# Kernel optimization log

Hardware: AMD Instinct MI355X
Metric: run time of the kernel (lower is better)

The kernel has to match this reference:

```python
import jax, jax.numpy as jnp
import numpy as np

N_NODES = 50000
N_EDGES = 600000
DIM = 128
N_LAYERS = 3
N_GRAPHS = 512
BN_EPS = 1e-5


def setup_inputs() -> dict:
    key = jax.random.key(0)
    ks = jax.random.split(key, 8)
    x = jax.random.normal(ks[0], (N_NODES, DIM), dtype=jnp.float32)
    edge_index = jax.random.randint(ks[1], (2, N_EDGES), 0, N_NODES, dtype=jnp.int32)
    batch = jnp.sort(jax.random.randint(ks[2], (N_NODES,), 0, N_GRAPHS, dtype=jnp.int32))
    W1s = jax.random.normal(ks[3], (N_LAYERS, DIM, DIM), dtype=jnp.float32) * (1.0 / np.sqrt(DIM))
    b1s = jnp.zeros((N_LAYERS, DIM), dtype=jnp.float32)
    W2s = jax.random.normal(ks[4], (N_LAYERS, DIM, DIM), dtype=jnp.float32) * (1.0 / np.sqrt(DIM))
    b2s = jnp.zeros((N_LAYERS, DIM), dtype=jnp.float32)
    gammas = jnp.ones((N_LAYERS, DIM), dtype=jnp.float32)
    betas = jnp.zeros((N_LAYERS, DIM), dtype=jnp.float32)
    return {"x": x, "edge_index": edge_index, "batch": batch,
            "W1s": W1s, "b1s": b1s, "W2s": W2s, "b2s": b2s,
            "gammas": gammas, "betas": betas}


def reference(x, edge_index, batch, W1s, b1s, W2s, b2s, gammas, betas):
    # EncoderGIN.forward: stack of GINConv (eps=0) -> ReLU -> BatchNorm1d (train mode),
    # then global_add_pool per layer and concat along feature dim.
    n_nodes = x.shape[0]
    src, dst = edge_index[0], edge_index[1]
    h = x
    pools = []
    for i in range(N_LAYERS):
        # GINConv: aggregate sum of neighbor feats at dst, add (1+0)*self
        agg = jax.ops.segment_sum(h[src], dst, num_segments=n_nodes) + h
        # MLP: Linear -> ReLU -> Linear
        h1 = jax.nn.relu(agg @ W1s[i] + b1s[i])
        h2 = h1 @ W2s[i] + b2s[i]
        # outer ReLU
        h2 = jax.nn.relu(h2)
        # BatchNorm1d, training mode (biased variance over the node dim)
        mean = jnp.mean(h2, axis=0)
        var = jnp.var(h2, axis=0)
        h = (h2 - mean) * jax.lax.rsqrt(var + BN_EPS) * gammas[i] + betas[i]
        pools.append(jax.ops.segment_sum(h, batch, num_segments=N_GRAPHS))
    return jnp.concatenate(pools, axis=1)  # [N_GRAPHS, N_LAYERS*DIM]
```

## Files before the change

kernel.cpp:

```cpp
#include <hip/hip_runtime.h>

#define N_NODES 50000
#define N_EDGES 600000
#define DIM 128
#define N_GRAPHS 512
#define N_LAYERS 3
#define OUT_STRIDE (N_LAYERS * DIM)
#define BN_EPS 1e-5f
#define N_REP 16
#define CAP 64

#define NPB 128
#define NBIN 391
#define BCAP_BIN 3072
#define PADC 16
#define EPB 4096
#define NB3 147

typedef __attribute__((ext_vector_type(8))) short short8;
typedef __attribute__((ext_vector_type(4))) float floatx4;

__device__ inline short f2bf(float f) {
    union { float f; unsigned u; } x{f};
    unsigned r = x.u + 0x7fffu + ((x.u >> 16) & 1u);
    return (short)(r >> 16);
}
__device__ inline float bf2f(short h) {
    union { unsigned u; float f; } x;
    x.u = ((unsigned)(unsigned short)h) << 16;
    return x.f;
}
__device__ inline void split_trunc(float f, short& hi, short& lo) {
    union { float f; unsigned u; } x{f};
    hi = (short)(x.u >> 16);
    union { unsigned u; float f; } hf;
    hf.u = x.u & 0xffff0000u;
    union { float f; unsigned u; } y{f - hf.f};
    lo = (short)(y.u >> 16);
}
__device__ inline floatx4 bf4_to_f4(uint2 w) {
    union { unsigned u; float f; } a, b, c, d;
    a.u = w.x << 16;
    b.u = w.x & 0xffff0000u;
    c.u = w.y << 16;
    d.u = w.y & 0xffff0000u;
    return floatx4{a.f, b.f, c.f, d.f};
}

__global__ __launch_bounds__(256) void prep_scatter_kernel(const int* __restrict__ src,
                                                           const int* __restrict__ dst,
                                                           int* __restrict__ binCur,
                                                           int2* __restrict__ binned,
                                                           const float* __restrict__ W1s,
                                                           const float* __restrict__ W2s,
                                                           short* __restrict__ Whi,
                                                           short* __restrict__ Wlo,
                                                           const float* __restrict__ x,
                                                           short* __restrict__ xb) {
    if (blockIdx.x < NB3) {
        __shared__ int hist[NBIN];
        __shared__ int basev[NBIN];
        const int t = threadIdx.x;
        for (int b = t; b < NBIN; b += 256) hist[b] = 0;
        __syncthreads();
        const int e0 = blockIdx.x * EPB;
        int sreg[16], dreg[16], rreg[16];
#pragma unroll
        for (int k = 0; k < 16; ++k) {
            int e = e0 + k * 256 + t;
            if (e < N_EDGES) {
                sreg[k] = src[e];
                dreg[k] = dst[e];
            } else {
                dreg[k] = -1;
            }
        }
#pragma unroll
        for (int k = 0; k < 16; ++k)
            if (dreg[k] >= 0) rreg[k] = atomicAdd(&hist[dreg[k] >> 7], 1);
        __syncthreads();
        for (int b = t; b < NBIN; b += 256) {
            int c = hist[b];
            basev[b] = (c > 0) ? atomicAdd(&binCur[b * PADC], c) : 0;
        }
        __syncthreads();
#pragma unroll
        for (int k = 0; k < 16; ++k)
            if (dreg[k] >= 0) {
                int b = dreg[k] >> 7;
                int pos = basev[b] + rreg[k];
                if (pos < BCAP_BIN)
                    binned[(size_t)b * BCAP_BIN + pos] = make_int2(sreg[k], dreg[k] & (NPB - 1));
            }
        return;
    }
    int i = (blockIdx.x - NB3) * 256 + threadIdx.x;
    if (i < 6 * DIM * DIM) {
        int mat = i >> 14;
        int e = i & 16383;
        int k = e >> 7, n = e & 127;
        const float* W = (mat < 3) ? (W1s + (size_t)mat * DIM * DIM)
                                   : (W2s + (size_t)(mat - 3) * DIM * DIM);
        float w = W[e];
        short hi = f2bf(w);
        short lo = f2bf(w - bf2f(hi));
        size_t o = ((size_t)mat << 14) + n * DIM + k;
        Whi[o] = hi;
        Wlo[o] = lo;
    }
    if (i < N_NODES * 32) {
        float4 v = ((const float4*)x)[i];
        unsigned lo = (unsigned short)f2bf(v.x) | ((unsigned)(unsigned short)f2bf(v.y) << 16);
        unsigned hi = (unsigned short)f2bf(v.z) | ((unsigned)(unsigned short)f2bf(v.w) << 16);
        ((uint2*)xb)[i] = make_uint2(lo, hi);
    }
}

__global__ __launch_bounds__(256) void bucket_build_kernel(const int* __restrict__ binCur,
                                                           const int2* __restrict__ binned,
                                                           int* __restrict__ deg,
                                                           int* __restrict__ esrc) {
    __shared__ int ldeg[NPB];
    __shared__ int lbuck[NPB * CAP];
    const int b = blockIdx.x;
    const int t = threadIdx.x;
    if (t < NPB) ldeg[t] = 0;
    __syncthreads();
    int n = binCur[b * PADC];
    if (n > BCAP_BIN) n = BCAP_BIN;
    const int2* bp = binned + (size_t)b * BCAP_BIN;
    for (int i = t; i < n; i += 256) {
        int2 e = bp[i];
        int slot = atomicAdd(&ldeg[e.y], 1);
        if (slot < CAP) lbuck[(e.y << 6) + slot] = e.x;
    }
    __syncthreads();
    const int node0 = b * NPB;
    const int nvalid = min(NPB, N_NODES - node0);
    if (t < NPB && t < nvalid) deg[node0 + t] = ldeg[t];
    const int nu4 = nvalid << 4;
    uint4* d4 = (uint4*)(esrc + ((size_t)node0 << 6));
    const uint4* s4 = (const uint4*)lbuck;
    for (int i = t; i < nu4; i += 256) d4[i] = s4[i];
}

__global__ __launch_bounds__(256, 6) void fused_layer_kernel(
    const short* __restrict__ hin,
    const int* __restrict__ deg,
    const int* __restrict__ esrc,
    const float* __restrict__ prevrep,
    const float* __restrict__ pgamma,
    const float* __restrict__ pbeta,
    const short* __restrict__ W1hi, const short* __restrict__ W1lo,
    const float* __restrict__ b1,
    const short* __restrict__ W2hi, const short* __restrict__ W2lo,
    const float* __restrict__ b2,
    const int* __restrict__ batch,
    short* __restrict__ out,
    float* __restrict__ srep,
    float* __restrict__ gout,
    int layer) {
    __shared__ unsigned sbuf[4096];
    __shared__ float GO_s[256];
    short* As_hi = (short*)sbuf;
    short* As_lo = (short*)(sbuf + 2048);
    const int tid = threadIdx.x;
    const int base = blockIdx.x * 32;

    if (prevrep) {
        float s = 0.f;
#pragma unroll
        for (int r = 0; r < N_REP; ++r) s += prevrep[r * 256 + tid];
        GO_s[tid] = s;
        __syncthreads();
        if (tid < 128) {
            const float invn = 1.0f / (float)N_NODES;
            float m = GO_s[tid] * invn;
            float var = GO_s[128 + tid] * invn - m * m;
            float G = pgamma[tid] * rsqrtf(var + BN_EPS);
            GO_s[tid] = G;
            GO_s[128 + tid] = pbeta[tid] - m * G;
        }
    } else {
        GO_s[tid] = (tid < 128) ? 1.f : 0.f;
    }
    __syncthreads();

    {
        const int hw = tid >> 5;
        const int l32 = tid & 31;
        floatx4 G4 = *(const floatx4*)&GO_s[4 * l32];
        floatx4 O4 = *(const floatx4*)&GO_s[128 + 4 * l32];
        const uint2* hb = (const uint2*)hin;
#pragma unroll
        for (int i = 0; i < 4; ++i) {
            int r = hw * 4 + i;
            int node = base + r;
            floatx4 acc = {0.f, 0.f, 0.f, 0.f};
            if (node < N_NODES) {
                acc = bf4_to_f4(hb[(size_t)node * 32 + l32]);
                int dgr = deg[node];
                if (dgr > CAP) dgr = CAP;
                int b = node << 6;
                int e = b + dgr;
                int j = b;
                for (; j + 8 <= e; j += 8) {
                    int s0 = esrc[j], s1 = esrc[j + 1], s2 = esrc[j + 2], s3 = esrc[j + 3];
                    int s4 = esrc[j + 4], s5 = esrc[j + 5], s6 = esrc[j + 6], s7 = esrc[j + 7];
                    uint2 w0 = hb[(size_t)s0 * 32 + l32];
                    uint2 w1 = hb[(size_t)s1 * 32 + l32];
                    uint2 w2 = hb[(size_t)s2 * 32 + l32];
                    uint2 w3 = hb[(size_t)s3 * 32 + l32];
                    uint2 w4 = hb[(size_t)s4 * 32 + l32];
                    uint2 w5 = hb[(size_t)s5 * 32 + l32];
                    uint2 w6 = hb[(size_t)s6 * 32 + l32];
                    uint2 w7 = hb[(size_t)s7 * 32 + l32];
                    acc += ((bf4_to_f4(w0) + bf4_to_f4(w1)) + (bf4_to_f4(w2) + bf4_to_f4(w3))) +
                           ((bf4_to_f4(w4) + bf4_to_f4(w5)) + (bf4_to_f4(w6) + bf4_to_f4(w7)));
                }
                if (j + 4 <= e) {
                    int s0 = esrc[j], s1 = esrc[j + 1], s2 = esrc[j + 2], s3 = esrc[j + 3];
                    uint2 w0 = hb[(size_t)s0 * 32 + l32];
                    uint2 w1 = hb[(size_t)s1 * 32 + l32];
                    uint2 w2 = hb[(size_t)s2 * 32 + l32];
                    uint2 w3 = hb[(size_t)s3 * 32 + l32];
                    acc += (bf4_to_f4(w0) + bf4_to_f4(w1)) + (bf4_to_f4(w2) + bf4_to_f4(w3));
                    j += 4;
                }
                for (; j < e; ++j) acc += bf4_to_f4(hb[(size_t)esrc[j] * 32 + l32]);
                float dp1 = (float)(dgr + 1);
                acc = G4 * acc + dp1 * O4;
            }
            short hi[4], lo[4];
#pragma unroll
            for (int q = 0; q < 4; ++q) split_trunc(acc[q], hi[q], lo[q]);
            unsigned h0 = (unsigned short)hi[0] | ((unsigned)(unsigned short)hi[1] << 16);
            unsigned h1 = (unsigned short)hi[2] | ((unsigned)(unsigned short)hi[3] << 16);
            unsigned l0 = (unsigned short)lo[0] | ((unsigned)(unsigned short)lo[1] << 16);
            unsigned l1 = (unsigned short)lo[2] | ((unsigned)(unsigned short)lo[3] << 16);
            int ch = l32 >> 1, half = l32 & 1;
            int pos = r * 128 + ((ch ^ (r & 15)) * 8) + half * 4;
            *(uint2*)&As_hi[pos] = make_uint2(h0, h1);
            *(uint2*)&As_lo[pos] = make_uint2(l0, l1);
        }
    }
    __syncthreads();

    const int wave = tid >> 6;
    const int lane = tid & 63;
    const int l15 = lane & 15;
    const int quad = lane >> 4;

    floatx4 acc[2][2];
#pragma unroll
    for (int mi = 0; mi < 2; ++mi)
#pragma unroll
        for (int nl = 0; nl < 2; ++nl) acc[mi][nl] = floatx4{0.f, 0.f, 0.f, 0.f};
#pragma unroll
    for (int ks = 0; ks < 4; ++ks) {
        short8 ahi[2], alo[2], bhi[2], blo[2];
#pragma unroll
        for (int mi = 0; mi < 2; ++mi) {
            int row = mi * 16 + l15;
            int pos = row * 128 + (((ks * 4 + quad) ^ l15) * 8);
            ahi[mi] = *(const short8*)&As_hi[pos];
            alo[mi] = *(const short8*)&As_lo[pos];
        }
#pragma unroll
        for (int nl = 0; nl < 2; ++nl) {
            size_t p = (size_t)((wave * 2 + nl) * 16 + l15) * DIM + ks * 32 + quad * 8;
            bhi[nl] = *(const short8*)&W1hi[p];
            blo[nl] = *(const short8*)&W1lo[p];
        }
#pragma unroll
        for (int mi = 0; mi < 2; ++mi)
#pragma unroll
            for (int nl = 0; nl < 2; ++nl) {
                acc[mi][nl] = __builtin_amdgcn_mfma_f32_16x16x32_bf16(ahi[mi], bhi[nl], acc[mi][nl], 0, 0, 0);
                acc[mi][nl] = __builtin_amdgcn_mfma_f32_16x16x32_bf16(alo[mi], bhi[nl], acc[mi][nl], 0, 0, 0);
                acc[mi][nl] = __builtin_amdgcn_mfma_f32_16x16x32_bf16(ahi[mi], blo[nl], acc[mi][nl], 0, 0, 0);
            }
    }
    __syncthreads();

#pragma unroll
    for (int mi = 0; mi < 2; ++mi)
#pragma unroll
        for (int nl = 0; nl < 2; ++nl) {
            int col = (wave * 2 + nl) * 16 + l15;
            float bv = b1[col];
#pragma unroll
            for (int reg = 0; reg < 4; ++reg) {
                int row = mi * 16 + quad * 4 + reg;
                float v = fmaxf(acc[mi][nl][reg] + bv, 0.f);
                union { float f; unsigned u; } x{v};
                union { unsigned u; float f; } hf;
                hf.u = x.u & 0xffff0000u;
                union { float f; unsigned u; } y{v - hf.f};
                unsigned w = hf.u | (y.u >> 16);
                sbuf[row * 128 + ((((col >> 2) ^ (row & 31)) * 4) + (col & 3))] = w;
            }
        }
    __syncthreads();

    floatx4 acc2[2][2];
#pragma unroll
    for (int mi = 0; mi < 2; ++mi)
#pragma unroll
        for (int nl = 0; nl < 2; ++nl) acc2[mi][nl] = floatx4{0.f, 0.f, 0.f, 0.f};
#pragma unroll
    for (int ks = 0; ks < 4; ++ks) {
        short8 ahi2[2], alo2[2], bhi[2], blo[2];
#pragma unroll
        for (int mi = 0; mi < 2; ++mi) {
            int row = mi * 16 + l15;
            int c5 = ks * 8 + quad * 2;
            unsigned w[8];
            *(uint4*)&w[0] = *(const uint4*)&sbuf[row * 128 + ((c5 ^ (row & 31)) * 4)];
            *(uint4*)&w[4] = *(const uint4*)&sbuf[row * 128 + (((c5 + 1) ^ (row & 31)) * 4)];
#pragma unroll
            for (int j = 0; j < 8; ++j) {
                ahi2[mi][j] = (short)(w[j] >> 16);
                alo2[mi][j] = (short)(w[j] & 0xffffu);
            }
        }
#pragma unroll
        for (int nl = 0; nl < 2; ++nl) {
            size_t p = (size_t)((wave * 2 + nl) * 16 + l15) * DIM + ks * 32 + quad * 8;
            bhi[nl] = *(const short8*)&W2hi[p];
            blo[nl] = *(const short8*)&W2lo[p];
        }
#pragma unroll
        for (int mi = 0; mi < 2; ++mi)
#pragma unroll
            for (int nl = 0; nl < 2; ++nl) {
                acc2[mi][nl] = __builtin_amdgcn_mfma_f32_16x16x32_bf16(ahi2[mi], bhi[nl], acc2[mi][nl], 0, 0, 0);
                acc2[mi][nl] = __builtin_amdgcn_mfma_f32_16x16x32_bf16(alo2[mi], bhi[nl], acc2[mi][nl], 0, 0, 0);
                acc2[mi][nl] = __builtin_amdgcn_mfma_f32_16x16x32_bf16(ahi2[mi], blo[nl], acc2[mi][nl], 0, 0, 0);
            }
    }
    __syncthreads();

    float* pool_s = (float*)sbuf;
    float* ssum = (float*)sbuf + 384;
    float* ssq = (float*)sbuf + 512;

    const int g0 = batch[base];
    int idxr[2][4];
#pragma unroll
    for (int mi = 0; mi < 2; ++mi)
#pragma unroll
        for (int reg = 0; reg < 4; ++reg) {
            int row = base + mi * 16 + quad * 4 + reg;
            idxr[mi][reg] = (row < N_NODES) ? (batch[row] - g0) : -1;
        }

#pragma unroll
    for (int nl = 0; nl < 2; ++nl) {
        int col = (wave * 2 + nl) * 16 + l15;
        float bv = b2[col];
        float s_p = 0.f, q_p = 0.f, p0 = 0.f, p1 = 0.f, p2 = 0.f;
#pragma unroll
        for (int mi = 0; mi < 2; ++mi)
#pragma unroll
            for (int reg = 0; reg < 4; ++reg) {
                int idx = idxr[mi][reg];
                if (idx >= 0) {
                    int row = base + mi * 16 + quad * 4 + reg;
                    float v = fmaxf(acc2[mi][nl][reg] + bv, 0.f);
                    out[(size_t)row * DIM + col] = f2bf(v);
                    s_p += v;
                    q_p += v * v;
                    if (idx == 0) p0 += v;
                    else if (idx == 1) p1 += v;
                    else if (idx == 2) p2 += v;
                    else atomicAdd(&gout[(size_t)(g0 + idx) * OUT_STRIDE + layer * DIM + col], v);
                }
            }
        s_p += __shfl_xor(s_p, 16);
        s_p += __shfl_xor(s_p, 32);
        q_p += __shfl_xor(q_p, 16);
        q_p += __shfl_xor(q_p, 32);
        p0 += __shfl_xor(p0, 16);
        p0 += __shfl_xor(p0, 32);
        p1 += __shfl_xor(p1, 16);
        p1 += __shfl_xor(p1, 32);
        p2 += __shfl_xor(p2, 16);
        p2 += __shfl_xor(p2, 32);
        if (quad == 0) {
            ssum[col] = s_p;
            ssq[col] = q_p;
            pool_s[col] = p0;
            pool_s[128 + col] = p1;
            pool_s[256 + col] = p2;
        }
    }
    __syncthreads();

    float* srep_b = srep + (blockIdx.x & (N_REP - 1)) * 256;
    if (tid < 128)
        atomicAdd(&srep_b[tid], ssum[tid]);
    else
        atomicAdd(&srep_b[tid], ssq[tid - 128]);
    for (int i = tid; i < 384; i += 256) {
        int slot = i >> 7, col = i & 127;
        float pv = pool_s[slot * 128 + col];
        int g = g0 + slot;
        if (pv != 0.f && g < N_GRAPHS)
            atomicAdd(&gout[(size_t)g * OUT_STRIDE + layer * DIM + col], pv);
    }
}

__global__ __launch_bounds__(384) void finalize_kernel(const float* __restrict__ rep,
                                                       const float* __restrict__ gammas,
                                                       const float* __restrict__ betas,
                                                       const int* __restrict__ batch,
                                                       float* __restrict__ out) {
    __shared__ float cntf;
    int b = blockIdx.x;
    int t = threadIdx.x;
    if (t == 0) {
        int lo = 0, hi = N_NODES;
        while (lo < hi) {
            int m = (lo + hi) >> 1;
            if (batch[m] < b) lo = m + 1;
            else hi = m;
        }
        int lo2 = lo, hi2 = N_NODES;
        while (lo2 < hi2) {
            int m = (lo2 + hi2) >> 1;
            if (batch[m] < b + 1) lo2 = m + 1;
            else hi2 = m;
        }
        cntf = (float)(lo2 - lo);
    }
    __syncthreads();
    int l = t >> 7, c = t & 127;
    const float* rl = rep + (size_t)l * N_REP * 256;
    float s = 0.f, q = 0.f;
#pragma unroll
    for (int r = 0; r < N_REP; ++r) {
        s += rl[r * 256 + c];
        q += rl[r * 256 + 128 + c];
    }
    const float invn = 1.0f / (float)N_NODES;
    float m = s * invn;
    float var = q * invn - m * m;
    float G = gammas[l * DIM + c] * rsqrtf(var + BN_EPS);
    float OFF = betas[l * DIM + c] - m * G;
    size_t o = (size_t)b * OUT_STRIDE + t;
    out[o] = fmaf(G, out[o], cntf * OFF);
}

extern "C" void kernel_launch(void* const* d_in, const int* in_sizes, int n_in,
                              void* d_out, int out_size, void* d_ws, size_t ws_size,
                              hipStream_t stream) {
    const float* x = (const float*)d_in[0];
    const int* ei = (const int*)d_in[1];
    const int* srcp = ei;
    const int* dstp = ei + N_EDGES;
    const int* batch = (const int*)d_in[2];
    const float* W1s = (const float*)d_in[3];
    const float* b1s = (const float*)d_in[4];
    const float* W2s = (const float*)d_in[5];
    const float* b2s = (const float*)d_in[6];
    const float* gammas = (const float*)d_in[7];
    const float* betas = (const float*)d_in[8];
    float* out = (float*)d_out;

    const size_t NF = (size_t)N_NODES * DIM;
    short* hbufA = (short*)d_ws;
    short* hbufB = hbufA + NF;
    short* xb = hbufB + NF;
    short* whi = xb + NF;
    short* wlo = whi + 6 * DIM * DIM;
    float* stats_rep = (float*)(wlo + 6 * DIM * DIM);
    int* binCur = (int*)(stats_rep + 3 * N_REP * 256);
    int* deg = binCur + NBIN * PADC;
    int* esrc = deg + N_NODES;
    int2* binned = (int2*)hbufB;

    hipMemsetAsync(out, 0, (size_t)N_GRAPHS * OUT_STRIDE * sizeof(float), stream);
    hipMemsetAsync(stats_rep, 0,
                   (3 * N_REP * 256) * sizeof(float) + (NBIN * PADC) * sizeof(int), stream);

    prep_scatter_kernel<<<NB3 + (N_NODES * 32 + 255) / 256, 256, 0, stream>>>(
        srcp, dstp, binCur, binned, W1s, W2s, whi, wlo, x, xb);
    bucket_build_kernel<<<NBIN, 256, 0, stream>>>(binCur, binned, deg, esrc);

    const int nblk = (N_NODES + 31) / 32;
    const short* hin = xb;
    short* hout = hbufA;
    for (int layer = 0; layer < N_LAYERS; ++layer) {
        const float* prevrep =
            (layer == 0) ? nullptr : (stats_rep + (size_t)(layer - 1) * N_REP * 256);
        fused_layer_kernel<<<nblk, 256, 0, stream>>>(
            hin, deg, esrc, prevrep, gammas + (layer - 1) * DIM, betas + (layer - 1) * DIM,
            whi + ((size_t)layer << 14), wlo + ((size_t)layer << 14), b1s + layer * DIM,
            whi + ((size_t)(3 + layer) << 14), wlo + ((size_t)(3 + layer) << 14),
            b2s + layer * DIM, batch, hout, stats_rep + (size_t)layer * N_REP * 256, out, layer);
        hin = hout;
        hout = (hout == hbufA) ? hbufB : hbufA;
    }
    finalize_kernel<<<N_GRAPHS, 384, 0, stream>>>(stats_rep, gammas, betas, batch, out);
}
```

Baseline: 278.8 us.

## Prefetch neighbor indices up front and gather padded sentinel rows branch-free

Adds a zero sentinel row at index N_NODES to every feature buffer and fills empty neighbor slots with that sentinel. The fused layer kernel then loads each node's degree and its first 16 neighbor indices as uint4 vectors before the BN-stats prologue, so that load latency overlaps the reduction. It gathers those 16 rows unconditionally, with no degree-dependent tail loops, and processes higher degrees in vectorised chunks of 8. The cost is extra gathers of the zero row for low-degree nodes, more register pressure (launch bounds occupancy lowered from 6 to 4), and slightly larger buffers.

Result: slower. 285.2 us (+2.3%).

```diff
diff --git a/kernel.cpp b/kernel.cpp
--- a/kernel.cpp
+++ b/kernel.cpp
@@ -56,7 +56,9 @@
                                                            short* __restrict__ Whi,
                                                            short* __restrict__ Wlo,
                                                            const float* __restrict__ x,
-                                                           short* __restrict__ xb) {
+                                                           short* __restrict__ xb,
+                                                           short* __restrict__ hbA,
+                                                           short* __restrict__ hbB) {
     if (blockIdx.x < NB3) {
         __shared__ int hist[NBIN];
         __shared__ int basev[NBIN];
@@ -113,6 +115,10 @@
         unsigned lo = (unsigned short)f2bf(v.x) | ((unsigned)(unsigned short)f2bf(v.y) << 16);
         unsigned hi = (unsigned short)f2bf(v.z) | ((unsigned)(unsigned short)f2bf(v.w) << 16);
         ((uint2*)xb)[i] = make_uint2(lo, hi);
+    } else if (i < (N_NODES + 1) * 32) {
+        ((uint2*)xb)[i] = make_uint2(0u, 0u);
+        ((uint2*)hbA)[i] = make_uint2(0u, 0u);
+        ((uint2*)hbB)[i] = make_uint2(0u, 0u);
     }
 }
 
@@ -124,6 +130,7 @@
     __shared__ int lbuck[NPB * CAP];
     const int b = blockIdx.x;
     const int t = threadIdx.x;
+    for (int i = t; i < NPB * CAP; i += 256) lbuck[i] = N_NODES;
     if (t < NPB) ldeg[t] = 0;
     __syncthreads();
     int n = binCur[b * PADC];
@@ -144,7 +151,7 @@
     for (int i = t; i < nu4; i += 256) d4[i] = s4[i];
 }
 
-__global__ __launch_bounds__(256, 6) void fused_layer_kernel(
+__global__ __launch_bounds__(256, 4) void fused_layer_kernel(
     const short* __restrict__ hin,
     const int* __restrict__ deg,
     const int* __restrict__ esrc,
@@ -167,6 +174,20 @@
     const int tid = threadIdx.x;
     const int base = blockIdx.x * 32;
 
+    const int hw = tid >> 5;
+    const int l32 = tid & 31;
+    int dgr_r[4];
+    uint4 idx_r[4][4];
+#pragma unroll
+    for (int i = 0; i < 4; ++i) {
+        int node = base + hw * 4 + i;
+        int nc = (node < N_NODES) ? node : (N_NODES - 1);
+        dgr_r[i] = deg[nc];
+        const uint4* ep = (const uint4*)(esrc + ((size_t)nc << 6));
+#pragma unroll
+        for (int q = 0; q < 4; ++q) idx_r[i][q] = ep[q];
+    }
+
     if (prevrep) {
         float s = 0.f;
 #pragma unroll
@@ -187,8 +208,6 @@
     __syncthreads();
 
     {
-        const int hw = tid >> 5;
-        const int l32 = tid & 31;
         floatx4 G4 = *(const floatx4*)&GO_s[4 * l32];
         floatx4 O4 = *(const floatx4*)&GO_s[128 + 4 * l32];
         const uint2* hb = (const uint2*)hin;
@@ -198,36 +217,41 @@
             int node = base + r;
             floatx4 acc = {0.f, 0.f, 0.f, 0.f};
             if (node < N_NODES) {
-                acc = bf4_to_f4(hb[(size_t)node * 32 + l32]);
-                int dgr = deg[node];
+                int dgr = dgr_r[i];
                 if (dgr > CAP) dgr = CAP;
-                int b = node << 6;
-                int e = b + dgr;
-                int j = b;
-                for (; j + 8 <= e; j += 8) {
-                    int s0 = esrc[j], s1 = esrc[j + 1], s2 = esrc[j + 2], s3 = esrc[j + 3];
-                    int s4 = esrc[j + 4], s5 = esrc[j + 5], s6 = esrc[j + 6], s7 = esrc[j + 7];
-                    uint2 w0 = hb[(size_t)s0 * 32 + l32];
-                    uint2 w1 = hb[(size_t)s1 * 32 + l32];
-                    uint2 w2 = hb[(size_t)s2 * 32 + l32];
-                    uint2 w3 = hb[(size_t)s3 * 32 + l32];
-                    uint2 w4 = hb[(size_t)s4 * 32 + l32];
-                    uint2 w5 = hb[(size_t)s5 * 32 + l32];
-                    uint2 w6 = hb[(size_t)s6 * 32 + l32];
-                    uint2 w7 = hb[(size_t)s7 * 32 + l32];
-                    acc += ((bf4_to_f4(w0) + bf4_to_f4(w1)) + (bf4_to_f4(w2) + bf4_to_f4(w3))) +
-                           ((bf4_to_f4(w4) + bf4_to_f4(w5)) + (bf4_to_f4(w6) + bf4_to_f4(w7)));
+                uint2 wv[16];
+                uint2 wself = hb[(size_t)node * 32 + l32];
+#pragma unroll
+                for (int q = 0; q < 4; ++q) {
+                    uint4 iq = idx_r[i][q];
+                    wv[4 * q + 0] = hb[(size_t)iq.x * 32 + l32];
+                    wv[4 * q + 1] = hb[(size_t)iq.y * 32 + l32];
+                    wv[4 * q + 2] = hb[(size_t)iq.z * 32 + l32];
+                    wv[4 * q + 3] = hb[(size_t)iq.w * 32 + l32];
                 }
-                if (j + 4 <= e) {
-                    int s0 = esrc[j], s1 = esrc[j + 1], s2 = esrc[j + 2], s3 = esrc[j + 3];
-                    uint2 w0 = hb[(size_t)s0 * 32 + l32];
-                    uint2 w1 = hb[(size_t)s1 * 32 + l32];
-                    uint2 w2 = hb[(size_t)s2 * 32 + l32];
-                    uint2 w3 = hb[(size_t)s3 * 32 + l32];
-                    acc += (bf4_to_f4(w0) + bf4_to_f4(w1)) + (bf4_to_f4(w2) + bf4_to_f4(w3));
-                    j += 4;
+                floatx4 t0 = (bf4_to_f4(wv[0]) + bf4_to_f4(wv[1])) + (bf4_to_f4(wv[2]) + bf4_to_f4(wv[3]));
+                floatx4 t1 = (bf4_to_f4(wv[4]) + bf4_to_f4(wv[5])) + (bf4_to_f4(wv[6]) + bf4_to_f4(wv[7]));
+                floatx4 t2 = (bf4_to_f4(wv[8]) + bf4_to_f4(wv[9])) + (bf4_to_f4(wv[10]) + bf4_to_f4(wv[11]));
+                floatx4 t3 = (bf4_to_f4(wv[12]) + bf4_to_f4(wv[13])) + (bf4_to_f4(wv[14]) + bf4_to_f4(wv[15]));
+                acc = bf4_to_f4(wself) + ((t0 + t1) + (t2 + t3));
+                if (dgr > 16) {
+                    int b0 = node << 6;
+                    int jend = b0 + ((dgr + 7) & ~7);
+                    for (int j = b0 + 16; j < jend; j += 8) {
+                        uint4 i0 = *(const uint4*)&esrc[j];
+                        uint4 i1 = *(const uint4*)&esrc[j + 4];
+                        uint2 w0 = hb[(size_t)i0.x * 32 + l32];
+                        uint2 w1 = hb[(size_t)i0.y * 32 + l32];
+                        uint2 w2 = hb[(size_t)i0.z * 32 + l32];
+                        uint2 w3 = hb[(size_t)i0.w * 32 + l32];
+                        uint2 w4 = hb[(size_t)i1.x * 32 + l32];
+                        uint2 w5 = hb[(size_t)i1.y * 32 + l32];
+                        uint2 w6 = hb[(size_t)i1.z * 32 + l32];
+                        uint2 w7 = hb[(size_t)i1.w * 32 + l32];
+                        acc += ((bf4_to_f4(w0) + bf4_to_f4(w1)) + (bf4_to_f4(w2) + bf4_to_f4(w3))) +
+                               ((bf4_to_f4(w4) + bf4_to_f4(w5)) + (bf4_to_f4(w6) + bf4_to_f4(w7)));
+                    }
                 }
-                for (; j < e; ++j) acc += bf4_to_f4(hb[(size_t)esrc[j] * 32 + l32]);
                 float dp1 = (float)(dgr + 1);
                 acc = G4 * acc + dp1 * O4;
             }
@@ -468,11 +492,11 @@
     const float* betas = (const float*)d_in[8];
     float* out = (float*)d_out;
 
-    const size_t NF = (size_t)N_NODES * DIM;
+    const size_t NFR = (size_t)(N_NODES + 1) * DIM;
     short* hbufA = (short*)d_ws;
-    short* hbufB = hbufA + NF;
-    short* xb = hbufB + NF;
-    short* whi = xb + NF;
+    short* hbufB = hbufA + NFR;
+    short* xb = hbufB + NFR;
+    short* whi = xb + NFR;
     short* wlo = whi + 6 * DIM * DIM;
     float* stats_rep = (float*)(wlo + 6 * DIM * DIM);
     int* binCur = (int*)(stats_rep + 3 * N_REP * 256);
@@ -484,8 +508,8 @@
     hipMemsetAsync(stats_rep, 0,
                    (3 * N_REP * 256) * sizeof(float) + (NBIN * PADC) * sizeof(int), stream);
 
-    prep_scatter_kernel<<<NB3 + (N_NODES * 32 + 255) / 256, 256, 0, stream>>>(
-        srcp, dstp, binCur, binned, W1s, W2s, whi, wlo, x, xb);
+    prep_scatter_kernel<<<NB3 + ((N_NODES + 1) * 32 + 255) / 256, 256, 0, stream>>>(
+        srcp, dstp, binCur, binned, W1s, W2s, whi, wlo, x, xb, hbufA, hbufB);
     bucket_build_kernel<<<NBIN, 256, 0, stream>>>(binCur, binned, deg, esrc);
 
     const int nblk = (N_NODES + 31) / 32;
```

## Replace global atomics for BN stats and pooling with per-tile partials plus reductions

Applied to the files above, without the earlier changes.

The fused layer kernel now writes per-block BatchNorm sums and squares and per-tile pooling partials (four graph slots) to workspace instead of doing global atomicAdds. A small reduce kernel folds the stat partials after each layer, and the finalize kernel gathers the pooling partials per graph by scanning the tiles that overlap it. Edge buckets are padded with a dummy zero node (N_NODES) and a zero row is added to the feature buffers, presumably so the gather loop can avoid bounds checks. This adds three extra kernel launches and more global traffic in exchange for removing atomic contention.

Result: slower. 363.2 us (+30.3%).

```diff
diff --git a/kernel.cpp b/kernel.cpp
--- a/kernel.cpp
+++ b/kernel.cpp
@@ -17,6 +17,9 @@
 #define EPB 4096
 #define NB3 147
 
+#define NTILES 1563
+#define NSLOT 4
+
 typedef __attribute__((ext_vector_type(8))) short short8;
 typedef __attribute__((ext_vector_type(4))) float floatx4;
 
@@ -56,7 +59,9 @@
                                                            short* __restrict__ Whi,
                                                            short* __restrict__ Wlo,
                                                            const float* __restrict__ x,
-                                                           short* __restrict__ xb) {
+                                                           short* __restrict__ xb,
+                                                           short* __restrict__ hbA,
+                                                           short* __restrict__ hbB) {
     if (blockIdx.x < NB3) {
         __shared__ int hist[NBIN];
         __shared__ int basev[NBIN];
@@ -113,6 +118,10 @@
         unsigned lo = (unsigned short)f2bf(v.x) | ((unsigned)(unsigned short)f2bf(v.y) << 16);
         unsigned hi = (unsigned short)f2bf(v.z) | ((unsigned)(unsigned short)f2bf(v.w) << 16);
         ((uint2*)xb)[i] = make_uint2(lo, hi);
+    } else if (i < (N_NODES + 1) * 32) {
+        ((uint2*)xb)[i] = make_uint2(0u, 0u);
+        ((uint2*)hbA)[i] = make_uint2(0u, 0u);
+        ((uint2*)hbB)[i] = make_uint2(0u, 0u);
     }
 }
 
@@ -124,6 +133,7 @@
     __shared__ int lbuck[NPB * CAP];
     const int b = blockIdx.x;
     const int t = threadIdx.x;
+    for (int i = t; i < NPB * CAP; i += 256) lbuck[i] = N_NODES;
     if (t < NPB) ldeg[t] = 0;
     __syncthreads();
     int n = binCur[b * PADC];
@@ -157,7 +167,8 @@
     const float* __restrict__ b2,
     const int* __restrict__ batch,
     short* __restrict__ out,
-    float* __restrict__ srep,
+    float* __restrict__ stats_part,
+    float* __restrict__ pool_part,
     float* __restrict__ gout,
     int layer) {
     __shared__ unsigned sbuf[4096];
@@ -342,8 +353,8 @@
     __syncthreads();
 
     float* pool_s = (float*)sbuf;
-    float* ssum = (float*)sbuf + 384;
-    float* ssq = (float*)sbuf + 512;
+    float* ssum = (float*)sbuf + NSLOT * 128;
+    float* ssq = (float*)sbuf + NSLOT * 128 + 128;
 
     const int g0 = batch[base];
     int idxr[2][4];
@@ -359,7 +370,7 @@
     for (int nl = 0; nl < 2; ++nl) {
         int col = (wave * 2 + nl) * 16 + l15;
         float bv = b2[col];
-        float s_p = 0.f, q_p = 0.f, p0 = 0.f, p1 = 0.f, p2 = 0.f;
+        float s_p = 0.f, q_p = 0.f, p0 = 0.f, p1 = 0.f, p2 = 0.f, p3 = 0.f;
 #pragma unroll
         for (int mi = 0; mi < 2; ++mi)
 #pragma unroll
@@ -374,6 +385,7 @@
                     if (idx == 0) p0 += v;
                     else if (idx == 1) p1 += v;
                     else if (idx == 2) p2 += v;
+                    else if (idx == 3) p3 += v;
                     else atomicAdd(&gout[(size_t)(g0 + idx) * OUT_STRIDE + layer * DIM + col], v);
                 }
             }
@@ -387,38 +399,43 @@
         p1 += __shfl_xor(p1, 32);
         p2 += __shfl_xor(p2, 16);
         p2 += __shfl_xor(p2, 32);
+        p3 += __shfl_xor(p3, 16);
+        p3 += __shfl_xor(p3, 32);
         if (quad == 0) {
             ssum[col] = s_p;
             ssq[col] = q_p;
             pool_s[col] = p0;
             pool_s[128 + col] = p1;
             pool_s[256 + col] = p2;
-        }
-    }
-    __syncthreads();
-
-    float* srep_b = srep + (blockIdx.x & (N_REP - 1)) * 256;
-    if (tid < 128)
-        atomicAdd(&srep_b[tid], ssum[tid]);
-    else
-        atomicAdd(&srep_b[tid], ssq[tid - 128]);
-    for (int i = tid; i < 384; i += 256) {
-        int slot = i >> 7, col = i & 127;
-        float pv = pool_s[slot * 128 + col];
-        int g = g0 + slot;
-        if (pv != 0.f && g < N_GRAPHS)
-            atomicAdd(&gout[(size_t)g * OUT_STRIDE + layer * DIM + col], pv);
-    }
+            pool_s[384 + col] = p3;
+        }
+    }
+    __syncthreads();
+
+    stats_part[(size_t)blockIdx.x * 256 + tid] = (tid < 128) ? ssum[tid] : ssq[tid - 128];
+    for (int i = tid; i < NSLOT * 128; i += 256)
+        pool_part[(size_t)blockIdx.x * (NSLOT * 128) + i] = pool_s[i];
+}
+
+__global__ __launch_bounds__(256) void reduce_stats_kernel(const float* __restrict__ sp,
+                                                           float* __restrict__ srep) {
+    const int r = blockIdx.x;
+    const int tid = threadIdx.x;
+    float s = 0.f;
+    for (int t = r; t < NTILES; t += N_REP) s += sp[(size_t)t * 256 + tid];
+    srep[r * 256 + tid] = s;
 }
 
 __global__ __launch_bounds__(384) void finalize_kernel(const float* __restrict__ rep,
+                                                       const float* __restrict__ pool_part,
                                                        const float* __restrict__ gammas,
                                                        const float* __restrict__ betas,
                                                        const int* __restrict__ batch,
                                                        float* __restrict__ out) {
     __shared__ float cntf;
-    int b = blockIdx.x;
-    int t = threadIdx.x;
+    __shared__ int stlo, sthi;
+    const int b = blockIdx.x;
+    const int t = threadIdx.x;
     if (t == 0) {
         int lo = 0, hi = N_NODES;
         while (lo < hi) {
@@ -433,9 +450,11 @@
             else hi2 = m;
         }
         cntf = (float)(lo2 - lo);
-    }
-    __syncthreads();
-    int l = t >> 7, c = t & 127;
+        stlo = lo >> 5;
+        sthi = (lo2 > lo) ? ((lo2 - 1) >> 5) : (lo >> 5) - 1;
+    }
+    __syncthreads();
+    const int l = t >> 7, c = t & 127;
     const float* rl = rep + (size_t)l * N_REP * 256;
     float s = 0.f, q = 0.f;
 #pragma unroll
@@ -448,8 +467,14 @@
     float var = q * invn - m * m;
     float G = gammas[l * DIM + c] * rsqrtf(var + BN_EPS);
     float OFF = betas[l * DIM + c] - m * G;
+    float ps = 0.f;
+    for (int tt = stlo; tt <= sthi; ++tt) {
+        int slot = b - batch[tt * 32];
+        if (slot >= 0 && slot < NSLOT)
+            ps += pool_part[((size_t)l * NTILES + tt) * (NSLOT * 128) + slot * 128 + c];
+    }
     size_t o = (size_t)b * OUT_STRIDE + t;
-    out[o] = fmaf(G, out[o], cntf * OFF);
+    out[o] = fmaf(G, out[o] + ps, cntf * OFF);
 }
 
 extern "C" void kernel_launch(void* const* d_in, const int* in_sizes, int n_in,
@@ -468,39 +493,42 @@
     const float* betas = (const float*)d_in[8];
     float* out = (float*)d_out;
 
-    const size_t NF = (size_t)N_NODES * DIM;
+    const size_t NFR = (size_t)(N_NODES + 1) * DIM;
     short* hbufA = (short*)d_ws;
-    short* hbufB = hbufA + NF;
-    short* xb = hbufB + NF;
-    short* whi = xb + NF;
+    short* hbufB = hbufA + NFR;
+    short* xb = hbufB + NFR;
+    short* whi = xb + NFR;
     short* wlo = whi + 6 * DIM * DIM;
     float* stats_rep = (float*)(wlo + 6 * DIM * DIM);
     int* binCur = (int*)(stats_rep + 3 * N_REP * 256);
     int* deg = binCur + NBIN * PADC;
     int* esrc = deg + N_NODES;
+    float* stats_part = (float*)(esrc + (size_t)N_NODES * CAP);
+    float* pool_part = stats_part + (size_t)NTILES * 256;
     int2* binned = (int2*)hbufB;
 
     hipMemsetAsync(out, 0, (size_t)N_GRAPHS * OUT_STRIDE * sizeof(float), stream);
-    hipMemsetAsync(stats_rep, 0,
-                   (3 * N_REP * 256) * sizeof(float) + (NBIN * PADC) * sizeof(int), stream);
-
-    prep_scatter_kernel<<<NB3 + (N_NODES * 32 + 255) / 256, 256, 0, stream>>>(
-        srcp, dstp, binCur, binned, W1s, W2s, whi, wlo, x, xb);
+    hipMemsetAsync(binCur, 0, (NBIN * PADC) * sizeof(int), stream);
+
+    prep_scatter_kernel<<<NB3 + ((N_NODES + 1) * 32 + 255) / 256, 256, 0, stream>>>(
+        srcp, dstp, binCur, binned, W1s, W2s, whi, wlo, x, xb, hbufA, hbufB);
     bucket_build_kernel<<<NBIN, 256, 0, stream>>>(binCur, binned, deg, esrc);
 
-    const int nblk = (N_NODES + 31) / 32;
     const short* hin = xb;
     short* hout = hbufA;
     for (int layer = 0; layer < N_LAYERS; ++layer) {
         const float* prevrep =
             (layer == 0) ? nullptr : (stats_rep + (size_t)(layer - 1) * N_REP * 256);
-        fused_layer_kernel<<<nblk, 256, 0, stream>>>(
+        fused_layer_kernel<<<NTILES, 256, 0, stream>>>(
             hin, deg, esrc, prevrep, gammas + (layer - 1) * DIM, betas + (layer - 1) * DIM,
             whi + ((size_t)layer << 14), wlo + ((size_t)layer << 14), b1s + layer * DIM,
             whi + ((size_t)(3 + layer) << 14), wlo + ((size_t)(3 + layer) << 14),
-            b2s + layer * DIM, batch, hout, stats_rep + (size_t)layer * N_REP * 256, out, layer);
+            b2s + layer * DIM, batch, hout, stats_part,
+            pool_part + (size_t)layer * NTILES * (NSLOT * 128), out, layer);
+        reduce_stats_kernel<<<N_REP, 256, 0, stream>>>(
+            stats_part, stats_rep + (size_t)layer * N_REP * 256);
         hin = hout;
         hout = (hout == hbufA) ? hbufB : hbufA;
     }
-    finalize_kernel<<<N_GRAPHS, 384, 0, stream>>>(stats_rep, gammas, betas, batch, out);
-}
+    finalize_kernel<<<N_GRAPHS, 384, 0, stream>>>(stats_rep, pool_part, gammas, betas, batch, out);
+}
```

## Shrink fused layer tile to 16 rows and drop bounds checks via zero pad row

Applied to the files above, without the earlier changes.

The fused GIN layer kernel now processes 16 nodes per block instead of 32, using 3125 blocks with half the shared memory and a launch bound allowing 8 blocks per CU, and each MFMA wave handles a single 16-row tile. A zero-filled padding node row is appended to the feature buffers and unused edge slots are filled with that index, so the per-node bounds checks in the gather and epilogue can go. The number of stat replicas is doubled to reduce atomic contention with the larger block count. The trade-off is that weight fragments are reloaded by twice as many blocks and the per-block prologue is repeated more often.

New measurement: 333.0 us. 1.19x slower.

```diff
diff --git a/kernel.cpp b/kernel.cpp
--- a/kernel.cpp
+++ b/kernel.cpp
@@ -7,7 +7,7 @@
 #define N_LAYERS 3
 #define OUT_STRIDE (N_LAYERS * DIM)
 #define BN_EPS 1e-5f
-#define N_REP 16
+#define N_REP 32
 #define CAP 64
 
 #define NPB 128
@@ -16,6 +16,9 @@
 #define PADC 16
 #define EPB 4096
 #define NB3 147
+
+#define TROWS 16
+#define NTILES 3125
 
 typedef __attribute__((ext_vector_type(8))) short short8;
 typedef __attribute__((ext_vector_type(4))) float floatx4;
@@ -56,7 +59,9 @@
                                                            short* __restrict__ Whi,
                                                            short* __restrict__ Wlo,
                                                            const float* __restrict__ x,
-                                                           short* __restrict__ xb) {
+                                                           short* __restrict__ xb,
+                                                           short* __restrict__ hbA,
+                                                           short* __restrict__ hbB) {
     if (blockIdx.x < NB3) {
         __shared__ int hist[NBIN];
         __shared__ int basev[NBIN];
@@ -113,6 +118,10 @@
         unsigned lo = (unsigned short)f2bf(v.x) | ((unsigned)(unsigned short)f2bf(v.y) << 16);
         unsigned hi = (unsigned short)f2bf(v.z) | ((unsigned)(unsigned short)f2bf(v.w) << 16);
         ((uint2*)xb)[i] = make_uint2(lo, hi);
+    } else if (i < (N_NODES + 1) * 32) {
+        ((uint2*)xb)[i] = make_uint2(0u, 0u);
+        ((uint2*)hbA)[i] = make_uint2(0u, 0u);
+        ((uint2*)hbB)[i] = make_uint2(0u, 0u);
     }
 }
 
@@ -124,6 +133,7 @@
     __shared__ int lbuck[NPB * CAP];
     const int b = blockIdx.x;
     const int t = threadIdx.x;
+    for (int i = t; i < NPB * CAP; i += 256) lbuck[i] = N_NODES;
     if (t < NPB) ldeg[t] = 0;
     __syncthreads();
     int n = binCur[b * PADC];
@@ -144,7 +154,7 @@
     for (int i = t; i < nu4; i += 256) d4[i] = s4[i];
 }
 
-__global__ __launch_bounds__(256, 6) void fused_layer_kernel(
+__global__ __launch_bounds__(256, 8) void fused_layer_kernel(
     const short* __restrict__ hin,
     const int* __restrict__ deg,
     const int* __restrict__ esrc,
@@ -160,12 +170,12 @@
     float* __restrict__ srep,
     float* __restrict__ gout,
     int layer) {
-    __shared__ unsigned sbuf[4096];
+    __shared__ unsigned sbuf[2048];
     __shared__ float GO_s[256];
     short* As_hi = (short*)sbuf;
-    short* As_lo = (short*)(sbuf + 2048);
+    short* As_lo = (short*)(sbuf + 1024);
     const int tid = threadIdx.x;
-    const int base = blockIdx.x * 32;
+    const int base = blockIdx.x * TROWS;
 
     if (prevrep) {
         float s = 0.f;
@@ -193,11 +203,11 @@
         floatx4 O4 = *(const floatx4*)&GO_s[128 + 4 * l32];
         const uint2* hb = (const uint2*)hin;
 #pragma unroll
-        for (int i = 0; i < 4; ++i) {
-            int r = hw * 4 + i;
+        for (int i = 0; i < 2; ++i) {
+            int r = hw * 2 + i;
             int node = base + r;
-            floatx4 acc = {0.f, 0.f, 0.f, 0.f};
-            if (node < N_NODES) {
+            floatx4 acc;
+            {
                 acc = bf4_to_f4(hb[(size_t)node * 32 + l32]);
                 int dgr = deg[node];
                 if (dgr > CAP) dgr = CAP;
@@ -239,7 +249,7 @@
             unsigned l0 = (unsigned short)lo[0] | ((unsigned)(unsigned short)lo[1] << 16);
             unsigned l1 = (unsigned short)lo[2] | ((unsigned)(unsigned short)lo[3] << 16);
             int ch = l32 >> 1, half = l32 & 1;
-            int pos = r * 128 + ((ch ^ (r & 15)) * 8) + half * 4;
+            int pos = r * 128 + ((ch ^ r) * 8) + half * 4;
             *(uint2*)&As_hi[pos] = make_uint2(h0, h1);
             *(uint2*)&As_lo[pos] = make_uint2(l0, l1);
         }
@@ -251,20 +261,17 @@
     const int l15 = lane & 15;
     const int quad = lane >> 4;
 
-    floatx4 acc[2][2];
-#pragma unroll
-    for (int mi = 0; mi < 2; ++mi)
-#pragma unroll
-        for (int nl = 0; nl < 2; ++nl) acc[mi][nl] = floatx4{0.f, 0.f, 0.f, 0.f};
+    floatx4 acc[2];
+#pragma unroll
+    for (int nl = 0; nl < 2; ++nl) acc[nl] = floatx4{0.f, 0.f, 0.f, 0.f};
 #pragma unroll
     for (int ks = 0; ks < 4; ++ks) {
-        short8 ahi[2], alo[2], bhi[2], blo[2];
-#pragma unroll
-        for (int mi = 0; mi < 2; ++mi) {
-            int row = mi * 16 + l15;
-            int pos = row * 128 + (((ks * 4 + quad) ^ l15) * 8);
-            ahi[mi] = *(const short8*)&As_hi[pos];
-            alo[mi] = *(const short8*)&As_lo[pos];
+        short8 ahi, alo, bhi[2], blo[2];
+        {
+            int row = l15;
+            int pos = row * 128 + (((ks * 4 + quad) ^ row) * 8);
+            ahi = *(const short8*)&As_hi[pos];
+            alo = *(const short8*)&As_lo[pos];
         }
 #pragma unroll
         for (int nl = 0; nl < 2; ++nl) {
@@ -273,55 +280,48 @@
             blo[nl] = *(const short8*)&W1lo[p];
         }
 #pragma unroll
-        for (int mi = 0; mi < 2; ++mi)
-#pragma unroll
-            for (int nl = 0; nl < 2; ++nl) {
-                acc[mi][nl] = __builtin_amdgcn_mfma_f32_16x16x32_bf16(ahi[mi], bhi[nl], acc[mi][nl], 0, 0, 0);
-                acc[mi][nl] = __builtin_amdgcn_mfma_f32_16x16x32_bf16(alo[mi], bhi[nl], acc[mi][nl], 0, 0, 0);
-                acc[mi][nl] = __builtin_amdgcn_mfma_f32_16x16x32_bf16(ahi[mi], blo[nl], acc[mi][nl], 0, 0, 0);
-            }
-    }
-    __syncthreads();
-
-#pragma unroll
-    for (int mi = 0; mi < 2; ++mi)
-#pragma unroll
         for (int nl = 0; nl < 2; ++nl) {
-            int col = (wave * 2 + nl) * 16 + l15;
-            float bv = b1[col];
-#pragma unroll
-            for (int reg = 0; reg < 4; ++reg) {
-                int row = mi * 16 + quad * 4 + reg;
-                float v = fmaxf(acc[mi][nl][reg] + bv, 0.f);
-                union { float f; unsigned u; } x{v};
-                union { unsigned u; float f; } hf;
-                hf.u = x.u & 0xffff0000u;
-                union { float f; unsigned u; } y{v - hf.f};
-                unsigned w = hf.u | (y.u >> 16);
-                sbuf[row * 128 + ((((col >> 2) ^ (row & 31)) * 4) + (col & 3))] = w;
-            }
-        }
-    __syncthreads();
-
-    floatx4 acc2[2][2];
-#pragma unroll
-    for (int mi = 0; mi < 2; ++mi)
-#pragma unroll
-        for (int nl = 0; nl < 2; ++nl) acc2[mi][nl] = floatx4{0.f, 0.f, 0.f, 0.f};
+            acc[nl] = __builtin_amdgcn_mfma_f32_16x16x32_bf16(ahi, bhi[nl], acc[nl], 0, 0, 0);
+            acc[nl] = __builtin_amdgcn_mfma_f32_16x16x32_bf16(alo, bhi[nl], acc[nl], 0, 0, 0);
+            acc[nl] = __builtin_amdgcn_mfma_f32_16x16x32_bf16(ahi, blo[nl], acc[nl], 0, 0, 0);
+        }
+    }
+    __syncthreads();
+
+#pragma unroll
+    for (int nl = 0; nl < 2; ++nl) {
+        int col = (wave * 2 + nl) * 16 + l15;
+        float bv = b1[col];
+#pragma unroll
+        for (int reg = 0; reg < 4; ++reg) {
+            int row = quad * 4 + reg;
+            float v = fmaxf(acc[nl][reg] + bv, 0.f);
+            union { float f; unsigned u; } x{v};
+            union { unsigned u; float f; } hf;
+            hf.u = x.u & 0xffff0000u;
+            union { float f; unsigned u; } y{v - hf.f};
+            unsigned w = hf.u | (y.u >> 16);
+            sbuf[row * 128 + ((((col >> 2) ^ row) * 4) + (col & 3))] = w;
+        }
+    }
+    __syncthreads();
+
+    floatx4 acc2[2];
+#pragma unroll
+    for (int nl = 0; nl < 2; ++nl) acc2[nl] = floatx4{0.f, 0.f, 0.f, 0.f};
 #pragma unroll
     for (int ks = 0; ks < 4; ++ks) {
-        short8 ahi2[2], alo2[2], bhi[2], blo[2];
-#pragma unroll
-        for (int mi = 0; mi < 2; ++mi) {
-            int row = mi * 16 + l15;
+        short8 ahi2, alo2, bhi[2], blo[2];
+        {
+            int row = l15;
             int c5 = ks * 8 + quad * 2;
             unsigned w[8];
-            *(uint4*)&w[0] = *(const uint4*)&sbuf[row * 128 + ((c5 ^ (row & 31)) * 4)];
-            *(uint4*)&w[4] = *(const uint4*)&sbuf[row * 128 + (((c5 + 1) ^ (row & 31)) * 4)];
+            *(uint4*)&w[0] = *(const uint4*)&sbuf[row * 128 + ((c5 ^ row) * 4)];
+            *(uint4*)&w[4] = *(const uint4*)&sbuf[row * 128 + (((c5 + 1) ^ row) * 4)];
 #pragma unroll
             for (int j = 0; j < 8; ++j) {
-                ahi2[mi][j] = (short)(w[j] >> 16);
-                alo2[mi][j] = (short)(w[j] & 0xffffu);
+                ahi2[j] = (short)(w[j] >> 16);
+                alo2[j] = (short)(w[j] & 0xffffu);
             }
         }
 #pragma unroll
@@ -331,13 +331,11 @@
             blo[nl] = *(const short8*)&W2lo[p];
         }
 #pragma unroll
-        for (int mi = 0; mi < 2; ++mi)
-#pragma unroll
-            for (int nl = 0; nl < 2; ++nl) {
-                acc2[mi][nl] = __builtin_amdgcn_mfma_f32_16x16x32_bf16(ahi2[mi], bhi[nl], acc2[mi][nl], 0, 0, 0);
-                acc2[mi][nl] = __builtin_amdgcn_mfma_f32_16x16x32_bf16(alo2[mi], bhi[nl], acc2[mi][nl], 0, 0, 0);
-                acc2[mi][nl] = __builtin_amdgcn_mfma_f32_16x16x32_bf16(ahi2[mi], blo[nl], acc2[mi][nl], 0, 0, 0);
-            }
+        for (int nl = 0; nl < 2; ++nl) {
+            acc2[nl] = __builtin_amdgcn_mfma_f32_16x16x32_bf16(ahi2, bhi[nl], acc2[nl], 0, 0, 0);
+            acc2[nl] = __builtin_amdgcn_mfma_f32_16x16x32_bf16(alo2, bhi[nl], acc2[nl], 0, 0, 0);
+            acc2[nl] = __builtin_amdgcn_mfma_f32_16x16x32_bf16(ahi2, blo[nl], acc2[nl], 0, 0, 0);
+        }
     }
     __syncthreads();
 
@@ -346,14 +344,12 @@
     float* ssq = (float*)sbuf + 512;
 
     const int g0 = batch[base];
-    int idxr[2][4];
-#pragma unroll
-    for (int mi = 0; mi < 2; ++mi)
-#pragma unroll
-        for (int reg = 0; reg < 4; ++reg) {
-            int row = base + mi * 16 + quad * 4 + reg;
-            idxr[mi][reg] = (row < N_NODES) ? (batch[row] - g0) : -1;
-        }
+    int idxr[4];
+#pragma unroll
+    for (int reg = 0; reg < 4; ++reg) {
+        int row = base + quad * 4 + reg;
+        idxr[reg] = batch[row] - g0;
+    }
 
 #pragma unroll
     for (int nl = 0; nl < 2; ++nl) {
@@ -361,22 +357,18 @@
         float bv = b2[col];
         float s_p = 0.f, q_p = 0.f, p0 = 0.f, p1 = 0.f, p2 = 0.f;
 #pragma unroll
-        for (int mi = 0; mi < 2; ++mi)
-#pragma unroll
-            for (int reg = 0; reg < 4; ++reg) {
-                int idx = idxr[mi][reg];
-                if (idx >= 0) {
-                    int row = base + mi * 16 + quad * 4 + reg;
-                    float v = fmaxf(acc2[mi][nl][reg] + bv, 0.f);
-                    out[(size_t)row * DIM + col] = f2bf(v);
-                    s_p += v;
-                    q_p += v * v;
-                    if (idx == 0) p0 += v;
-                    else if (idx == 1) p1 += v;
-                    else if (idx == 2) p2 += v;
-                    else atomicAdd(&gout[(size_t)(g0 + idx) * OUT_STRIDE + layer * DIM + col], v);
-                }
-            }
+        for (int reg = 0; reg < 4; ++reg) {
+            int idx = idxr[reg];
+            int row = base + quad * 4 + reg;
+            float v = fmaxf(acc2[nl][reg] + bv, 0.f);
+            out[(size_t)row * DIM + col] = f2bf(v);
+            s_p += v;
+            q_p += v * v;
+            if (idx == 0) p0 += v;
+            else if (idx == 1) p1 += v;
+            else if (idx == 2) p2 += v;
+            else atomicAdd(&gout[(size_t)(g0 + idx) * OUT_STRIDE + layer * DIM + col], v);
+        }
         s_p += __shfl_xor(s_p, 16);
         s_p += __shfl_xor(s_p, 32);
         q_p += __shfl_xor(q_p, 16);
@@ -468,11 +460,11 @@
     const float* betas = (const float*)d_in[8];
     float* out = (float*)d_out;
 
-    const size_t NF = (size_t)N_NODES * DIM;
+    const size_t NFR = (size_t)(N_NODES + 1) * DIM;
     short* hbufA = (short*)d_ws;
-    short* hbufB = hbufA + NF;
-    short* xb = hbufB + NF;
-    short* whi = xb + NF;
+    short* hbufB = hbufA + NFR;
+    short* xb = hbufB + NFR;
+    short* whi = xb + NFR;
     short* wlo = whi + 6 * DIM * DIM;
     float* stats_rep = (float*)(wlo + 6 * DIM * DIM);
     int* binCur = (int*)(stats_rep + 3 * N_REP * 256);
@@ -484,17 +476,16 @@
     hipMemsetAsync(stats_rep, 0,
                    (3 * N_REP * 256) * sizeof(float) + (NBIN * PADC) * sizeof(int), stream);
 
-    prep_scatter_kernel<<<NB3 + (N_NODES * 32 + 255) / 256, 256, 0, stream>>>(
-        srcp, dstp, binCur, binned, W1s, W2s, whi, wlo, x, xb);
+    prep_scatter_kernel<<<NB3 + ((N_NODES + 1) * 32 + 255) / 256, 256, 0, stream>>>(
+        srcp, dstp, binCur, binned, W1s, W2s, whi, wlo, x, xb, hbufA, hbufB);
     bucket_build_kernel<<<NBIN, 256, 0, stream>>>(binCur, binned, deg, esrc);
 
-    const int nblk = (N_NODES + 31) / 32;
     const short* hin = xb;
     short* hout = hbufA;
     for (int layer = 0; layer < N_LAYERS; ++layer) {
         const float* prevrep =
             (layer == 0) ? nullptr : (stats_rep + (size_t)(layer - 1) * N_REP * 256);
-        fused_layer_kernel<<<nblk, 256, 0, stream>>>(
+        fused_layer_kernel<<<NTILES, 256, 0, stream>>>(
             hin, deg, esrc, prevrep, gammas + (layer - 1) * DIM, betas + (layer - 1) * DIM,
             whi + ((size_t)layer << 14), wlo + ((size_t)layer << 14), b1s + layer * DIM,
             whi + ((size_t)(3 + layer) << 14), wlo + ((size_t)(3 + layer) << 14),
```
